# Kernel tuning notes

Measured on AMD Instinct MI355X. Metric: run time of the kernel, lower is better.

The kernel has to match this reference:

```python
import jax, jax.numpy as jnp
import numpy as np

B, S, D_MODEL, H, OUT = 32, 64, 256, 256, 10
N_POS = 64  # n_max_seq + 1


def _coordinate_map():
    i = jnp.arange(N_POS, dtype=jnp.float32)
    r = jnp.sqrt(jnp.float32(N_POS))
    c0 = (i / r - 2.0) / 2.0
    c1 = (jnp.mod(i, r) - 2.0) / 2.0
    coord = jnp.stack([c0, c1], axis=-1)            # [N_POS, 2]
    return jnp.broadcast_to(coord[None], (B, N_POS, 2))


def setup_inputs() -> dict:
    key = jax.random.key(0)
    ks = jax.random.split(key, 13)
    d_in = (D_MODEL + 2) * 3
    w = lambda k, i, o: jax.random.normal(k, (i, o), jnp.float32) * 0.02
    b = lambda k, o: jax.random.normal(k, (o,), jnp.float32) * 0.02
    return {
        'sentences': jax.random.normal(ks[0], (B, S, D_MODEL), jnp.float32),
        'coord': _coordinate_map(),
        'g_w1': w(ks[1], d_in, H), 'g_b1': b(ks[2], H),
        'g_w2': w(ks[3], H, H),    'g_b2': b(ks[4], H),
        'g_w3': w(ks[5], H, H),    'g_b3': b(ks[6], H),
        'f_w1': w(ks[7], H, H),    'f_b1': b(ks[8], H),
        'f_w2': w(ks[9], H, H),    'f_b2': b(ks[10], H),
        'f_w3': w(ks[11], H, OUT), 'f_b3': b(ks[12], OUT),
    }


def reference(sentences, coord, g_w1, g_b1, g_w2, g_b2, g_w3, g_b3,
              f_w1, f_b1, f_w2, f_b2, f_w3, f_b3):
    b, s, d = sentences.shape
    x = jnp.concatenate([sentences, coord[:b, :s, :]], axis=-1)   # [B,S,D+2]
    oi = jnp.broadcast_to(x[:, None, :, :], (b, s, s, d + 2))     # object_i[b,i,j]=x[b,j]
    oj = jnp.broadcast_to(x[:, :, None, :], (b, s, s, d + 2))     # object_j[b,i,j]=x[b,i]
    pairs = jnp.concatenate([oi, oj, oi * oj], axis=-1)           # [B,S,S,3*(D+2)]
    h = jax.nn.relu(jnp.einsum('bijk,kh->bijh', pairs, g_w1) + g_b1)
    h = jax.nn.relu(h @ g_w2 + g_b2)
    h = jax.nn.relu(h @ g_w3 + g_b3)
    rel = h.reshape(b, s * s, -1).sum(axis=1)                     # [B,H]
    y = jax.nn.relu(rel @ f_w1 + f_b1)
    y = jax.nn.relu(y @ f_w2 + f_b2)                              # Dropout: eval mode (identity)
    return y @ f_w3 + f_b3                                        # [B,OUT]
```

## Files before the change

kernel.cpp:

```cpp
#include <hip/hip_runtime.h>
#include <hip/hip_bf16.h>


typedef __attribute__((ext_vector_type(4))) float f32x4;
typedef __attribute__((ext_vector_type(16))) float f32x16;
typedef __attribute__((ext_vector_type(8))) short frag8;
typedef __attribute__((ext_vector_type(4))) unsigned u32x4;

__device__ __forceinline__ float bf2f(short s) {
  return __uint_as_float(((unsigned)(unsigned short)s) << 16);
}
__device__ __forceinline__ short f2bf(float f) {
  unsigned u = __float_as_uint(f);
  return (short)((u + 0x7fffu + ((u >> 16) & 1u)) >> 16);
}

__device__ __forceinline__ unsigned pk_bf16(float lo, float hi) {
#if __has_builtin(__builtin_amdgcn_cvt_pk_bf16_f32)
  return __builtin_bit_cast(unsigned, __builtin_amdgcn_cvt_pk_bf16_f32(lo, hi));
#else
  unsigned ul = __float_as_uint(lo), uh = __float_as_uint(hi);
  ul = (ul + 0x7fffu + ((ul >> 16) & 1u)) >> 16;
  uh = (uh + 0x7fffu + ((uh >> 16) & 1u)) & 0xffff0000u;
  return ul | uh;
#endif
}

__device__ __forceinline__ unsigned pk_mul_bf16(unsigned a, unsigned b) {
  float al = __uint_as_float(a << 16);
  float ah = __uint_as_float(a & 0xffff0000u);
  float bl = __uint_as_float(b << 16);
  float bh = __uint_as_float(b & 0xffff0000u);
  return pk_bf16(al * bl, ah * bh);
}

__device__ __forceinline__ frag8 pk_mul4(u32x4 a, u32x4 b) {
  u32x4 r;
#pragma unroll
  for (int t = 0; t < 4; t++) r[t] = pk_mul_bf16(a[t], b[t]);
  return __builtin_bit_cast(frag8, r);
}

#define KX 288
#define KS 272

__global__ __launch_bounds__(256)
void prep(const float* __restrict__ sent, const float* __restrict__ coord,
          const float* __restrict__ g_w1, const float* __restrict__ g_w2,
          const float* __restrict__ g_w3,
          short* __restrict__ xb, short* __restrict__ Wab, short* __restrict__ Wc,
          short* __restrict__ W2t, short* __restrict__ W3t, float* __restrict__ rel) {
  __shared__ short tile[64 * 66];
  const int blk = blockIdx.x, t = threadIdx.x;

  if (blk < 288) {
    long idx0 = ((long)blk * 256 + t) * 8;
#pragma unroll
    for (int e = 0; e < 8; e++) {
      long idx = idx0 + e;
      int row = (int)(idx / KX), k = (int)(idx - (long)row * KX);
      float v = 0.f;
      if (k < 256)      v = sent[(size_t)row * 256 + k];
      else if (k < 258) v = coord[row * 2 + (k - 256)];
      xb[idx] = f2bf(v);
    }
    return;
  }

  const int nc = t & 63, r4 = t >> 6;
  if (blk < 328) {
    int tt = blk - 288, kt = tt >> 3, nt = tt & 7;
    int k0 = kt * 64, n0 = nt * 64;
    for (int p = 0; p < 16; p++) {
      int kl = p * 4 + r4, k = k0 + kl, n = n0 + nc;
      float v = 0.f;
      if (k < 258) {
        int row = (n < 256) ? k : 258 + k;
        int col = (n < 256) ? n : n - 256;
        v = g_w1[(size_t)row * 256 + col];
      }
      tile[kl * 66 + nc] = f2bf(v);
    }
    __syncthreads();
    for (int p = 0; p < 16; p++) {
      int nl = p * 4 + r4;
      if (k0 + nc < KX) Wab[(size_t)(n0 + nl) * KX + k0 + nc] = tile[nc * 66 + nl];
    }
    return;
  }
  if (blk < 348) {
    int tt = blk - 328, kt = tt >> 2, nt = tt & 3;
    int k0 = kt * 64, n0 = nt * 64;
    for (int p = 0; p < 16; p++) {
      int kl = p * 4 + r4, k = k0 + kl;
      float v = (k < 258) ? g_w1[(size_t)(516 + k) * 256 + n0 + nc] : 0.f;
      tile[kl * 66 + nc] = f2bf(v);
    }
    __syncthreads();
    for (int p = 0; p < 16; p++) {
      int nl = p * 4 + r4;
      if (k0 + nc < KX) Wc[(size_t)(n0 + nl) * KX + k0 + nc] = tile[nc * 66 + nl];
    }
    return;
  }
  if (blk < 380) {
    int tt = blk - 348;
    const float* W = (tt < 16) ? g_w2 : g_w3;
    short* Wt = (tt < 16) ? W2t : W3t;
    tt &= 15;
    int k0 = (tt >> 2) * 64, n0 = (tt & 3) * 64;
    for (int p = 0; p < 16; p++) {
      int kl = p * 4 + r4;
      tile[kl * 66 + nc] = f2bf(W[(size_t)(k0 + kl) * 256 + n0 + nc]);
    }
    __syncthreads();
    for (int p = 0; p < 16; p++) {
      int nl = p * 4 + r4;
      Wt[(size_t)(n0 + nl) * 256 + k0 + nc] = tile[nc * 66 + nl];
    }
    return;
  }
  {
    int bb = blk - 380;
    ((f32x4*)rel)[bb * 256 + t] = (f32x4){0.f, 0.f, 0.f, 0.f};
  }
}


__global__ __launch_bounds__(64)
void uv_gemm(const short* __restrict__ xb, const short* __restrict__ Wab,
             const float* __restrict__ g_b1, float* __restrict__ uT,
             float* __restrict__ vbuf) {
  const int m0 = blockIdx.x * 64;
  const int n0 = blockIdx.y * 64;
  const int lane = threadIdx.x;
  const int q = lane >> 4, l16 = lane & 15;

  f32x4 acc[4][4];
#pragma unroll
  for (int mt = 0; mt < 4; mt++)
#pragma unroll
    for (int nt = 0; nt < 4; nt++) acc[mt][nt] = (f32x4){0.f, 0.f, 0.f, 0.f};

  for (int k0 = 0; k0 < KX; k0 += 32) {
    frag8 a[4], bb[4];
#pragma unroll
    for (int mt = 0; mt < 4; mt++)
      a[mt] = *(const frag8*)(xb + (size_t)(m0 + mt * 16 + l16) * KX + k0 + q * 8);
#pragma unroll
    for (int nt = 0; nt < 4; nt++)
      bb[nt] = *(const frag8*)(Wab + (size_t)(n0 + nt * 16 + l16) * KX + k0 + q * 8);
#pragma unroll
    for (int mt = 0; mt < 4; mt++)
#pragma unroll
      for (int nt = 0; nt < 4; nt++)
        acc[mt][nt] = __builtin_amdgcn_mfma_f32_16x16x32_bf16(a[mt], bb[nt], acc[mt][nt], 0, 0, 0);
  }
  if (n0 < 256) {
#pragma unroll
    for (int nt = 0; nt < 4; nt++) {
      int col = n0 + nt * 16 + l16;
#pragma unroll
      for (int mt = 0; mt < 4; mt++)
        *(f32x4*)(uT + ((size_t)blockIdx.x * 256 + col) * 64 + mt * 16 + q * 4) = acc[mt][nt];
    }
  } else {
#pragma unroll
    for (int nt = 0; nt < 4; nt++) {
      int c = n0 - 256 + nt * 16 + l16;
      float bias = g_b1[c];
#pragma unroll
      for (int mt = 0; mt < 4; mt++) {
        int m = m0 + mt * 16 + q * 4;
#pragma unroll
        for (int r = 0; r < 4; r++)
          vbuf[(size_t)(m + r) * 256 + c] = acc[mt][nt][r] + bias;
      }
    }
  }
}


#define ASH 280
#define LDS_SHORTS (128 * ASH)

__global__ __launch_bounds__(256, 2)
void relnet_main(const short* __restrict__ xb, const short* __restrict__ Wc,
                 const short* __restrict__ W2t, const short* __restrict__ W3t,
                 const float* __restrict__ uT, const float* __restrict__ vbuf,
                 const float* __restrict__ g_b2, const float* __restrict__ g_b3,
                 float* __restrict__ rel) {
  __shared__ short lds[LDS_SHORTS];

  const int tid = threadIdx.x;
  const int bi = blockIdx.x;
  const int b = bi >> 5, ip = bi & 31;
  const int i0 = ip * 2;
  const int lane = tid & 63, wave = tid >> 6;
  const int l32 = lane & 31, half = lane >> 5;
  const int n0 = wave * 64;
  const int rowbase = b * 64;
  const int swr = l32 & 7;

  f32x16 acc[4][2];
#pragma unroll
  for (int mt = 0; mt < 4; mt++)
#pragma unroll
    for (int nt = 0; nt < 2; nt++)
#pragma unroll
      for (int r = 0; r < 16; r++) acc[mt][nt][r] = 0.f;

#pragma unroll
  for (int it = 0; it < 17; it++) {
    int idx = tid + it * 256;
    int j = idx / 34, c = idx - j * 34;
    int k = c * 8;
    u32x4 aj = *(const u32x4*)(xb + (size_t)(rowbase + (j & 63)) * KX + k);
    u32x4 ai = *(const u32x4*)(xb + (size_t)(rowbase + i0 + (j >> 6)) * KX + k);
    *(frag8*)(&lds[j * ASH + k]) = pk_mul4(aj, ai);
  }

  const short* wc0 = Wc + (size_t)(n0 + l32) * KX + half * 8;
  const short* wc1 = Wc + (size_t)(n0 + 32 + l32) * KX + half * 8;
  frag8 bp[2][2];
  bp[0][0] = *(const frag8*)(wc0);
  bp[0][1] = *(const frag8*)(wc1);
  bp[1][0] = *(const frag8*)(wc0 + 16);
  bp[1][1] = *(const frag8*)(wc1 + 16);
  __syncthreads();

#pragma unroll
  for (int ks = 0; ks < 17; ks++) {
    frag8 bc0 = bp[ks & 1][0], bc1 = bp[ks & 1][1];
    if (ks + 2 < 17) {
      bp[ks & 1][0] = *(const frag8*)(wc0 + (ks + 2) * 16);
      bp[ks & 1][1] = *(const frag8*)(wc1 + (ks + 2) * 16);
    }
    frag8 a[4];
#pragma unroll
    for (int mt = 0; mt < 4; mt++)
      a[mt] = *(const frag8*)(&lds[(mt * 32 + l32) * ASH + ks * 16 + half * 8]);
#pragma unroll
    for (int mt = 0; mt < 4; mt++) {
      acc[mt][0] = __builtin_amdgcn_mfma_f32_32x32x16_bf16(a[mt], bc0, acc[mt][0], 0, 0, 0);
      acc[mt][1] = __builtin_amdgcn_mfma_f32_32x32x16_bf16(a[mt], bc1, acc[mt][1], 0, 0, 0);
    }
  }
  __syncthreads();

  {
#pragma unroll
    for (int nt = 0; nt < 2; nt++) {
      int col = n0 + nt * 32 + l32;
      int cb = (n0 + nt * 32) >> 3;
      const float* ubp = uT + ((size_t)b * 256 + col) * 64;
      float vv0 = vbuf[(size_t)(rowbase + i0) * 256 + col];
      float vv1 = vbuf[(size_t)(rowbase + i0 + 1) * 256 + col];
#pragma unroll
      for (int mt = 0; mt < 4; mt++) {
        float vv = (mt < 2) ? vv0 : vv1;
#pragma unroll
        for (int r = 0; r < 16; r += 2) {
          int rb0 = (r & 3) + 8 * (r >> 2) + 4 * half;
          int jm0 = (mt & 1) * 32 + rb0;
          float2 uu = *(const float2*)(ubp + jm0);
          float x0 = fmaxf(acc[mt][nt][r]     + uu.x + vv, 0.f);
          float x1 = fmaxf(acc[mt][nt][r + 1] + uu.y + vv, 0.f);
          unsigned pk = pk_bf16(x0, x1);
          int m0r = mt * 32 + rb0;
          int sw0 = (r & 3) + 4 * half;
          lds[m0r * 256 + (((cb + (l32 >> 3)) ^ sw0) << 3) + (l32 & 7)] = (short)(pk & 0xffffu);
          lds[(m0r + 1) * 256 + (((cb + (l32 >> 3)) ^ (sw0 + 1)) << 3) + (l32 & 7)] = (short)(pk >> 16);
        }
#pragma unroll
        for (int r = 0; r < 16; r++) acc[mt][nt][r] = 0.f;
      }
    }
  }
  const short* w20 = W2t + (size_t)(n0 + l32) * 256 + half * 8;
  const short* w21 = W2t + (size_t)(n0 + 32 + l32) * 256 + half * 8;
  bp[0][0] = *(const frag8*)(w20);
  bp[0][1] = *(const frag8*)(w21);
  bp[1][0] = *(const frag8*)(w20 + 16);
  bp[1][1] = *(const frag8*)(w21 + 16);
  __syncthreads();

#pragma unroll
  for (int ks = 0; ks < 16; ks++) {
    frag8 bc0 = bp[ks & 1][0], bc1 = bp[ks & 1][1];
    if (ks + 2 < 16) {
      bp[ks & 1][0] = *(const frag8*)(w20 + (ks + 2) * 16);
      bp[ks & 1][1] = *(const frag8*)(w21 + (ks + 2) * 16);
    }
    frag8 a[4];
#pragma unroll
    for (int mt = 0; mt < 4; mt++)
      a[mt] = *(const frag8*)(&lds[(mt * 32 + l32) * 256 + (((2 * ks + half) ^ swr) << 3)]);
#pragma unroll
    for (int mt = 0; mt < 4; mt++) {
      acc[mt][0] = __builtin_amdgcn_mfma_f32_32x32x16_bf16(a[mt], bc0, acc[mt][0], 0, 0, 0);
      acc[mt][1] = __builtin_amdgcn_mfma_f32_32x32x16_bf16(a[mt], bc1, acc[mt][1], 0, 0, 0);
    }
  }
  __syncthreads();

#pragma unroll
  for (int nt = 0; nt < 2; nt++) {
    int col = n0 + nt * 32 + l32;
    int cb = (n0 + nt * 32) >> 3;
    float b2 = g_b2[col];
#pragma unroll
    for (int mt = 0; mt < 4; mt++) {
#pragma unroll
      for (int r = 0; r < 16; r += 2) {
        int rb0 = (r & 3) + 8 * (r >> 2) + 4 * half;
        float x0 = fmaxf(acc[mt][nt][r] + b2, 0.f);
        float x1 = fmaxf(acc[mt][nt][r + 1] + b2, 0.f);
        unsigned pk = pk_bf16(x0, x1);
        int m0r = mt * 32 + rb0;
        int sw0 = (r & 3) + 4 * half;
        lds[m0r * 256 + (((cb + (l32 >> 3)) ^ sw0) << 3) + (l32 & 7)] = (short)(pk & 0xffffu);
        lds[(m0r + 1) * 256 + (((cb + (l32 >> 3)) ^ (sw0 + 1)) << 3) + (l32 & 7)] = (short)(pk >> 16);
      }
#pragma unroll
      for (int r = 0; r < 16; r++) acc[mt][nt][r] = 0.f;
    }
  }
  const short* w30 = W3t + (size_t)(n0 + l32) * 256 + half * 8;
  const short* w31 = W3t + (size_t)(n0 + 32 + l32) * 256 + half * 8;
  bp[0][0] = *(const frag8*)(w30);
  bp[0][1] = *(const frag8*)(w31);
  bp[1][0] = *(const frag8*)(w30 + 16);
  bp[1][1] = *(const frag8*)(w31 + 16);
  __syncthreads();

#pragma unroll
  for (int ks = 0; ks < 16; ks++) {
    frag8 bc0 = bp[ks & 1][0], bc1 = bp[ks & 1][1];
    if (ks + 2 < 16) {
      bp[ks & 1][0] = *(const frag8*)(w30 + (ks + 2) * 16);
      bp[ks & 1][1] = *(const frag8*)(w31 + (ks + 2) * 16);
    }
    frag8 a[4];
#pragma unroll
    for (int mt = 0; mt < 4; mt++)
      a[mt] = *(const frag8*)(&lds[(mt * 32 + l32) * 256 + (((2 * ks + half) ^ swr) << 3)]);
#pragma unroll
    for (int mt = 0; mt < 4; mt++) {
      acc[mt][0] = __builtin_amdgcn_mfma_f32_32x32x16_bf16(a[mt], bc0, acc[mt][0], 0, 0, 0);
      acc[mt][1] = __builtin_amdgcn_mfma_f32_32x32x16_bf16(a[mt], bc1, acc[mt][1], 0, 0, 0);
    }
  }
#pragma unroll
  for (int nt = 0; nt < 2; nt++) {
    int col = n0 + nt * 32 + l32;
    float b3 = g_b3[col];
    float s = 0.f;
#pragma unroll
    for (int mt = 0; mt < 4; mt++)
#pragma unroll
      for (int r = 0; r < 16; r++)
        s += fmaxf(acc[mt][nt][r] + b3, 0.f);
    s += __shfl_xor(s, 32, 64);
    if (half == 0) atomicAdd(&rel[b * 256 + col], s);
  }
}

__global__ __launch_bounds__(256)
void fnet(const float* __restrict__ rel, const float* __restrict__ f_w1,
          const float* __restrict__ f_b1, const float* __restrict__ f_w2,
          const float* __restrict__ f_b2, const float* __restrict__ f_w3,
          const float* __restrict__ f_b3, float* __restrict__ out) {
  int b = blockIdx.x, t = threadIdx.x;
  __shared__ float y0[256], y1[256], y2[256];
  y0[t] = rel[b * 256 + t];
  __syncthreads();
  float s = f_b1[t];
#pragma unroll 8
  for (int k = 0; k < 256; k++) s += y0[k] * f_w1[k * 256 + t];
  y1[t] = fmaxf(s, 0.f);
  __syncthreads();
  s = f_b2[t];
#pragma unroll 8
  for (int k = 0; k < 256; k++) s += y1[k] * f_w2[k * 256 + t];
  y2[t] = fmaxf(s, 0.f);
  __syncthreads();
  if (t < 10) {
    float s2 = f_b3[t];
#pragma unroll 8
    for (int k = 0; k < 256; k++) s2 += y2[k] * f_w3[k * 10 + t];
    out[b * 10 + t] = s2;
  }
}

extern "C" void kernel_launch(void* const* d_in, const int* in_sizes, int n_in,
                              void* d_out, int out_size, void* d_ws, size_t ws_size,
                              hipStream_t stream) {
  const float* sent  = (const float*)d_in[0];
  const float* coord = (const float*)d_in[1];
  const float* g_w1  = (const float*)d_in[2];
  const float* g_b1  = (const float*)d_in[3];
  const float* g_w2  = (const float*)d_in[4];
  const float* g_b2  = (const float*)d_in[5];
  const float* g_w3  = (const float*)d_in[6];
  const float* g_b3  = (const float*)d_in[7];
  const float* f_w1  = (const float*)d_in[8];
  const float* f_b1  = (const float*)d_in[9];
  const float* f_w2  = (const float*)d_in[10];
  const float* f_b2  = (const float*)d_in[11];
  const float* f_w3  = (const float*)d_in[12];
  const float* f_b3  = (const float*)d_in[13];
  float* out = (float*)d_out;

  char* ws = (char*)d_ws;
  size_t off = 0;
  auto alloc = [&](size_t bytes) {
    char* p = ws + off;
    off += (bytes + 255) & ~(size_t)255;
    return p;
  };
  short* xb   = (short*)alloc((size_t)2048 * KX * 2);
  short* Wab  = (short*)alloc((size_t)512 * KX * 2);
  short* Wc   = (short*)alloc((size_t)256 * KX * 2);
  short* W2t  = (short*)alloc((size_t)256 * 256 * 2);
  short* W3t  = (short*)alloc((size_t)256 * 256 * 2);
  float* uT   = (float*)alloc((size_t)32 * 256 * 64 * 4);
  float* vbuf = (float*)alloc((size_t)2048 * 256 * 4);
  float* rel  = (float*)alloc((size_t)32 * 256 * 4);

  prep<<<388, 256, 0, stream>>>(sent, coord, g_w1, g_w2, g_w3, xb, Wab, Wc, W2t, W3t, rel);
  uv_gemm<<<dim3(32, 8), 64, 0, stream>>>(xb, Wab, g_b1, uT, vbuf);
  relnet_main<<<1024, 256, 0, stream>>>(xb, Wc, W2t, W3t, uT, vbuf, g_b2, g_b3, rel);
  fnet<<<32, 256, 0, stream>>>(rel, f_w1, f_b1, f_w2, f_b2, f_w3, f_b3, out);
}
```

Baseline: 217.5 us.

## Split first-layer A staging into two halves and merge u/v buffers

The first GEMM's product-feature staging in LDS is split into two halves along K, so the second half is built after the first half's MFMAs are issued. This lets global loads and packing overlap with compute instead of all preceding it. The u and v outputs are merged into one row-major [2048,512] buffer, and the B-fragment prefetch becomes a triple-buffered register ring. In exchange, the u reads in the epilogue become strided scalar loads instead of float2 loads, and an extra barrier is added.

```diff
diff --git a/kernel.cpp b/kernel.cpp
--- a/kernel.cpp
+++ b/kernel.cpp
@@ -42,7 +42,6 @@
 }
 
 #define KX 288
-#define KS 272
 
 __global__ __launch_bounds__(256)
 void prep(const float* __restrict__ sent, const float* __restrict__ coord,
@@ -129,8 +128,7 @@
 
 __global__ __launch_bounds__(64)
 void uv_gemm(const short* __restrict__ xb, const short* __restrict__ Wab,
-             const float* __restrict__ g_b1, float* __restrict__ uT,
-             float* __restrict__ vbuf) {
+             const float* __restrict__ g_b1, float* __restrict__ uv) {
   const int m0 = blockIdx.x * 64;
   const int n0 = blockIdx.y * 64;
   const int lane = threadIdx.x;
@@ -156,40 +154,30 @@
       for (int nt = 0; nt < 4; nt++)
         acc[mt][nt] = __builtin_amdgcn_mfma_f32_16x16x32_bf16(a[mt], bb[nt], acc[mt][nt], 0, 0, 0);
   }
-  if (n0 < 256) {
-#pragma unroll
-    for (int nt = 0; nt < 4; nt++) {
-      int col = n0 + nt * 16 + l16;
-#pragma unroll
-      for (int mt = 0; mt < 4; mt++)
-        *(f32x4*)(uT + ((size_t)blockIdx.x * 256 + col) * 64 + mt * 16 + q * 4) = acc[mt][nt];
-    }
-  } else {
-#pragma unroll
-    for (int nt = 0; nt < 4; nt++) {
-      int c = n0 - 256 + nt * 16 + l16;
-      float bias = g_b1[c];
-#pragma unroll
-      for (int mt = 0; mt < 4; mt++) {
-        int m = m0 + mt * 16 + q * 4;
-#pragma unroll
-        for (int r = 0; r < 4; r++)
-          vbuf[(size_t)(m + r) * 256 + c] = acc[mt][nt][r] + bias;
-      }
-    }
-  }
-}
-
-
-#define ASH 280
-#define LDS_SHORTS (128 * ASH)
+#pragma unroll
+  for (int nt = 0; nt < 4; nt++) {
+    int col = n0 + nt * 16 + l16;
+    float bias = (col >= 256) ? g_b1[col - 256] : 0.f;
+#pragma unroll
+    for (int mt = 0; mt < 4; mt++) {
+      int m = m0 + mt * 16 + q * 4;
+#pragma unroll
+      for (int r = 0; r < 4; r++)
+        uv[(size_t)(m + r) * 512 + col] = acc[mt][nt][r] + bias;
+    }
+  }
+}
+
+
+#define ASH 156
+#define A2OFF (128 * ASH)
+#define LDS_SHORTS (2 * 128 * ASH)
 
 __global__ __launch_bounds__(256, 2)
 void relnet_main(const short* __restrict__ xb, const short* __restrict__ Wc,
                  const short* __restrict__ W2t, const short* __restrict__ W3t,
-                 const float* __restrict__ uT, const float* __restrict__ vbuf,
-                 const float* __restrict__ g_b2, const float* __restrict__ g_b3,
-                 float* __restrict__ rel) {
+                 const float* __restrict__ uv, const float* __restrict__ g_b2,
+                 const float* __restrict__ g_b3, float* __restrict__ rel) {
   __shared__ short lds[LDS_SHORTS];
 
   const int tid = threadIdx.x;
@@ -211,9 +199,9 @@
       for (int r = 0; r < 16; r++) acc[mt][nt][r] = 0.f;
 
 #pragma unroll
-  for (int it = 0; it < 17; it++) {
+  for (int it = 0; it < 9; it++) {
     int idx = tid + it * 256;
-    int j = idx / 34, c = idx - j * 34;
+    int j = idx / 18, c = idx - j * 18;
     int k = c * 8;
     u32x4 aj = *(const u32x4*)(xb + (size_t)(rowbase + (j & 63)) * KX + k);
     u32x4 ai = *(const u32x4*)(xb + (size_t)(rowbase + i0 + (j >> 6)) * KX + k);
@@ -222,19 +210,18 @@
 
   const short* wc0 = Wc + (size_t)(n0 + l32) * KX + half * 8;
   const short* wc1 = Wc + (size_t)(n0 + 32 + l32) * KX + half * 8;
-  frag8 bp[2][2];
-  bp[0][0] = *(const frag8*)(wc0);
-  bp[0][1] = *(const frag8*)(wc1);
-  bp[1][0] = *(const frag8*)(wc0 + 16);
-  bp[1][1] = *(const frag8*)(wc1 + 16);
-  __syncthreads();
-
-#pragma unroll
-  for (int ks = 0; ks < 17; ks++) {
-    frag8 bc0 = bp[ks & 1][0], bc1 = bp[ks & 1][1];
+  frag8 bq0[3], bq1[3];
+  bq0[0] = *(const frag8*)(wc0);
+  bq1[0] = *(const frag8*)(wc1);
+  bq0[1] = *(const frag8*)(wc0 + 16);
+  bq1[1] = *(const frag8*)(wc1 + 16);
+  __syncthreads();
+
+#pragma unroll
+  for (int ks = 0; ks < 9; ks++) {
     if (ks + 2 < 17) {
-      bp[ks & 1][0] = *(const frag8*)(wc0 + (ks + 2) * 16);
-      bp[ks & 1][1] = *(const frag8*)(wc1 + (ks + 2) * 16);
+      bq0[(ks + 2) % 3] = *(const frag8*)(wc0 + (ks + 2) * 16);
+      bq1[(ks + 2) % 3] = *(const frag8*)(wc1 + (ks + 2) * 16);
     }
     frag8 a[4];
 #pragma unroll
@@ -242,20 +229,49 @@
       a[mt] = *(const frag8*)(&lds[(mt * 32 + l32) * ASH + ks * 16 + half * 8]);
 #pragma unroll
     for (int mt = 0; mt < 4; mt++) {
-      acc[mt][0] = __builtin_amdgcn_mfma_f32_32x32x16_bf16(a[mt], bc0, acc[mt][0], 0, 0, 0);
-      acc[mt][1] = __builtin_amdgcn_mfma_f32_32x32x16_bf16(a[mt], bc1, acc[mt][1], 0, 0, 0);
+      acc[mt][0] = __builtin_amdgcn_mfma_f32_32x32x16_bf16(a[mt], bq0[ks % 3], acc[mt][0], 0, 0, 0);
+      acc[mt][1] = __builtin_amdgcn_mfma_f32_32x32x16_bf16(a[mt], bq1[ks % 3], acc[mt][1], 0, 0, 0);
+    }
+  }
+
+#pragma unroll
+  for (int it = 0; it < 8; it++) {
+    int idx = tid + it * 256;
+    int j = idx >> 4, c = idx & 15;
+    int k = 144 + c * 8;
+    u32x4 aj = *(const u32x4*)(xb + (size_t)(rowbase + (j & 63)) * KX + k);
+    u32x4 ai = *(const u32x4*)(xb + (size_t)(rowbase + i0 + (j >> 6)) * KX + k);
+    *(frag8*)(&lds[A2OFF + j * ASH + c * 8]) = pk_mul4(aj, ai);
+  }
+  __syncthreads();
+
+#pragma unroll
+  for (int ks = 9; ks < 17; ks++) {
+    if (ks + 2 < 17) {
+      bq0[(ks + 2) % 3] = *(const frag8*)(wc0 + (ks + 2) * 16);
+      bq1[(ks + 2) % 3] = *(const frag8*)(wc1 + (ks + 2) * 16);
+    }
+    frag8 a[4];
+#pragma unroll
+    for (int mt = 0; mt < 4; mt++)
+      a[mt] = *(const frag8*)(&lds[A2OFF + (mt * 32 + l32) * ASH + (ks - 9) * 16 + half * 8]);
+#pragma unroll
+    for (int mt = 0; mt < 4; mt++) {
+      acc[mt][0] = __builtin_amdgcn_mfma_f32_32x32x16_bf16(a[mt], bq0[ks % 3], acc[mt][0], 0, 0, 0);
+      acc[mt][1] = __builtin_amdgcn_mfma_f32_32x32x16_bf16(a[mt], bq1[ks % 3], acc[mt][1], 0, 0, 0);
     }
   }
   __syncthreads();
 
   {
+    const float* ub = uv + (size_t)rowbase * 512;
+    const float* v0p = uv + (size_t)(rowbase + i0) * 512 + 256;
+    const float* v1p = uv + (size_t)(rowbase + i0 + 1) * 512 + 256;
 #pragma unroll
     for (int nt = 0; nt < 2; nt++) {
       int col = n0 + nt * 32 + l32;
       int cb = (n0 + nt * 32) >> 3;
-      const float* ubp = uT + ((size_t)b * 256 + col) * 64;
-      float vv0 = vbuf[(size_t)(rowbase + i0) * 256 + col];
-      float vv1 = vbuf[(size_t)(rowbase + i0 + 1) * 256 + col];
+      float vv0 = v0p[col], vv1 = v1p[col];
 #pragma unroll
       for (int mt = 0; mt < 4; mt++) {
         float vv = (mt < 2) ? vv0 : vv1;
@@ -263,9 +279,8 @@
         for (int r = 0; r < 16; r += 2) {
           int rb0 = (r & 3) + 8 * (r >> 2) + 4 * half;
           int jm0 = (mt & 1) * 32 + rb0;
-          float2 uu = *(const float2*)(ubp + jm0);
-          float x0 = fmaxf(acc[mt][nt][r]     + uu.x + vv, 0.f);
-          float x1 = fmaxf(acc[mt][nt][r + 1] + uu.y + vv, 0.f);
+          float x0 = fmaxf(acc[mt][nt][r]     + ub[(size_t)jm0 * 512 + col] + vv, 0.f);
+          float x1 = fmaxf(acc[mt][nt][r + 1] + ub[(size_t)(jm0 + 1) * 512 + col] + vv, 0.f);
           unsigned pk = pk_bf16(x0, x1);
           int m0r = mt * 32 + rb0;
           int sw0 = (r & 3) + 4 * half;
@@ -279,18 +294,17 @@
   }
   const short* w20 = W2t + (size_t)(n0 + l32) * 256 + half * 8;
   const short* w21 = W2t + (size_t)(n0 + 32 + l32) * 256 + half * 8;
-  bp[0][0] = *(const frag8*)(w20);
-  bp[0][1] = *(const frag8*)(w21);
-  bp[1][0] = *(const frag8*)(w20 + 16);
-  bp[1][1] = *(const frag8*)(w21 + 16);
+  bq0[0] = *(const frag8*)(w20);
+  bq1[0] = *(const frag8*)(w21);
+  bq0[1] = *(const frag8*)(w20 + 16);
+  bq1[1] = *(const frag8*)(w21 + 16);
   __syncthreads();
 
 #pragma unroll
   for (int ks = 0; ks < 16; ks++) {
-    frag8 bc0 = bp[ks & 1][0], bc1 = bp[ks & 1][1];
     if (ks + 2 < 16) {
-      bp[ks & 1][0] = *(const frag8*)(w20 + (ks + 2) * 16);
-      bp[ks & 1][1] = *(const frag8*)(w21 + (ks + 2) * 16);
+      bq0[(ks + 2) % 3] = *(const frag8*)(w20 + (ks + 2) * 16);
+      bq1[(ks + 2) % 3] = *(const frag8*)(w21 + (ks + 2) * 16);
     }
     frag8 a[4];
 #pragma unroll
@@ -298,8 +312,8 @@
       a[mt] = *(const frag8*)(&lds[(mt * 32 + l32) * 256 + (((2 * ks + half) ^ swr) << 3)]);
 #pragma unroll
     for (int mt = 0; mt < 4; mt++) {
-      acc[mt][0] = __builtin_amdgcn_mfma_f32_32x32x16_bf16(a[mt], bc0, acc[mt][0], 0, 0, 0);
-      acc[mt][1] = __builtin_amdgcn_mfma_f32_32x32x16_bf16(a[mt], bc1, acc[mt][1], 0, 0, 0);
+      acc[mt][0] = __builtin_amdgcn_mfma_f32_32x32x16_bf16(a[mt], bq0[ks % 3], acc[mt][0], 0, 0, 0);
+      acc[mt][1] = __builtin_amdgcn_mfma_f32_32x32x16_bf16(a[mt], bq1[ks % 3], acc[mt][1], 0, 0, 0);
     }
   }
   __syncthreads();
@@ -328,18 +342,17 @@
   }
   const short* w30 = W3t + (size_t)(n0 + l32) * 256 + half * 8;
   const short* w31 = W3t + (size_t)(n0 + 32 + l32) * 256 + half * 8;
-  bp[0][0] = *(const frag8*)(w30);
-  bp[0][1] = *(const frag8*)(w31);
-  bp[1][0] = *(const frag8*)(w30 + 16);
-  bp[1][1] = *(const frag8*)(w31 + 16);
+  bq0[0] = *(const frag8*)(w30);
+  bq1[0] = *(const frag8*)(w31);
+  bq0[1] = *(const frag8*)(w30 + 16);
+  bq1[1] = *(const frag8*)(w31 + 16);
   __syncthreads();
 
 #pragma unroll
   for (int ks = 0; ks < 16; ks++) {
-    frag8 bc0 = bp[ks & 1][0], bc1 = bp[ks & 1][1];
     if (ks + 2 < 16) {
-      bp[ks & 1][0] = *(const frag8*)(w30 + (ks + 2) * 16);
-      bp[ks & 1][1] = *(const frag8*)(w31 + (ks + 2) * 16);
+      bq0[(ks + 2) % 3] = *(const frag8*)(w30 + (ks + 2) * 16);
+      bq1[(ks + 2) % 3] = *(const frag8*)(w31 + (ks + 2) * 16);
     }
     frag8 a[4];
 #pragma unroll
@@ -347,8 +360,8 @@
       a[mt] = *(const frag8*)(&lds[(mt * 32 + l32) * 256 + (((2 * ks + half) ^ swr) << 3)]);
 #pragma unroll
     for (int mt = 0; mt < 4; mt++) {
-      acc[mt][0] = __builtin_amdgcn_mfma_f32_32x32x16_bf16(a[mt], bc0, acc[mt][0], 0, 0, 0);
-      acc[mt][1] = __builtin_amdgcn_mfma_f32_32x32x16_bf16(a[mt], bc1, acc[mt][1], 0, 0, 0);
+      acc[mt][0] = __builtin_amdgcn_mfma_f32_32x32x16_bf16(a[mt], bq0[ks % 3], acc[mt][0], 0, 0, 0);
+      acc[mt][1] = __builtin_amdgcn_mfma_f32_32x32x16_bf16(a[mt], bq1[ks % 3], acc[mt][1], 0, 0, 0);
     }
   }
 #pragma unroll
@@ -419,17 +432,16 @@
     off += (bytes + 255) & ~(size_t)255;
     return p;
   };
-  short* xb   = (short*)alloc((size_t)2048 * KX * 2);
-  short* Wab  = (short*)alloc((size_t)512 * KX * 2);
-  short* Wc   = (short*)alloc((size_t)256 * KX * 2);
-  short* W2t  = (short*)alloc((size_t)256 * 256 * 2);
-  short* W3t  = (short*)alloc((size_t)256 * 256 * 2);
-  float* uT   = (float*)alloc((size_t)32 * 256 * 64 * 4);
-  float* vbuf = (float*)alloc((size_t)2048 * 256 * 4);
-  float* rel  = (float*)alloc((size_t)32 * 256 * 4);
+  short* xb  = (short*)alloc((size_t)2048 * KX * 2);
+  short* Wab = (short*)alloc((size_t)512 * KX * 2);
+  short* Wc  = (short*)alloc((size_t)256 * KX * 2);
+  short* W2t = (short*)alloc((size_t)256 * 256 * 2);
+  short* W3t = (short*)alloc((size_t)256 * 256 * 2);
+  float* uv  = (float*)alloc((size_t)2048 * 512 * 4);
+  float* rel = (float*)alloc((size_t)32 * 256 * 4);
 
   prep<<<388, 256, 0, stream>>>(sent, coord, g_w1, g_w2, g_w3, xb, Wab, Wc, W2t, W3t, rel);
-  uv_gemm<<<dim3(32, 8), 64, 0, stream>>>(xb, Wab, g_b1, uT, vbuf);
-  relnet_main<<<1024, 256, 0, stream>>>(xb, Wc, W2t, W3t, uT, vbuf, g_b2, g_b3, rel);
+  uv_gemm<<<dim3(32, 8), 64, 0, stream>>>(xb, Wab, g_b1, uv);
+  relnet_main<<<1024, 256, 0, stream>>>(xb, Wc, W2t, W3t, uv, g_b2, g_b3, rel);
   fnet<<<32, 256, 0, stream>>>(rel, f_w1, f_b1, f_w2, f_b2, f_w3, f_b3, out);
 }
```

Result: faster. 183.8 us, median of 2 (-15.5%).
